# Kernel optimization log

Hardware: AMD Instinct MI355X
Metric: run time of the kernel (lower is better)

The kernel has to match this reference:

```python
import jax, jax.numpy as jnp
import numpy as np

NUM_HIDDENS = 512
NUM_HEADS = 4
B, S = 4, 2048


def setup_inputs() -> dict:
    key = jax.random.key(0)
    ks = jax.random.split(key, 10)
    H = NUM_HIDDENS
    scale = 1.0 / np.sqrt(H)
    return {
        "queries": jax.random.normal(ks[0], (B, S, H), jnp.float32),
        "keys": jax.random.normal(ks[1], (B, S, H), jnp.float32),
        "values": jax.random.normal(ks[2], (B, S, H), jnp.float32),
        "attention_mask": jax.random.randint(ks[3], (B, S), 0, 2).astype(bool),
        "Wq": jax.random.normal(ks[4], (H, H), jnp.float32) * scale,
        "bq": jnp.zeros((H,), jnp.float32),
        "Wk": jax.random.normal(ks[5], (H, H), jnp.float32) * scale,
        "bk": jnp.zeros((H,), jnp.float32),
        "Wv": jax.random.normal(ks[6], (H, H), jnp.float32) * scale,
        "bv": jnp.zeros((H,), jnp.float32),
    }


def reference(queries, keys, values, attention_mask, Wq, bq, Wk, bk, Wv, bv):
    B_, S_, H = queries.shape
    nh = NUM_HEADS
    dh = H // nh

    # QKV projections with ReLU (as in the original Sequential(Linear, ReLU))
    q = jax.nn.relu(jnp.einsum("bsh,oh->bso", queries, Wq) + bq)
    k = jax.nn.relu(jnp.einsum("bsh,oh->bso", keys, Wk) + bk)
    v = jax.nn.relu(jnp.einsum("bsh,oh->bso", values, Wv) + bv)

    # chunk along last dim + stack dim=1  ==  reshape [B,S,nh,dh] -> [B,nh,S,dh]
    qs = q.reshape(B_, S_, nh, dh).transpose(0, 2, 1, 3)
    ks_ = k.reshape(B_, S_, nh, dh).transpose(0, 2, 1, 3)
    vs = v.reshape(B_, S_, nh, dh).transpose(0, 2, 1, 3)

    # scores [B, nh, S, S]
    score = jnp.einsum("bhqd,bhkd->bhqk", qs, ks_) / jnp.sqrt(jnp.float32(dh))

    # 'enc' mask: [B,S] -> [B,1,S,1], fills entire QUERY rows (faithful quirk)
    row_mask = attention_mask[:, None, :, None]
    score = jnp.where(row_mask, jnp.float32(-1e9), score)

    attn = jax.nn.softmax(score, axis=-1)
    a = jnp.einsum("bhqk,bhkd->bhqd", attn, vs)  # [B, nh, S, dh]

    # faithful quirk: permute(0,1,3,2) then reshape to (B, S, H)
    a = jnp.transpose(a, (0, 1, 3, 2)).reshape(B_, S_, H)
    return a + queries
```

## Files before the change

### kernel.cpp

```cpp
#include <hip/hip_runtime.h>
#include <hip/hip_bf16.h>

typedef __attribute__((ext_vector_type(8)))  __bf16 bf16x8;
typedef __attribute__((ext_vector_type(4)))  __bf16 bf16x4;
typedef __attribute__((ext_vector_type(2)))  __bf16 bf16x2;
typedef __attribute__((ext_vector_type(4)))  float  f32x4;
typedef __attribute__((ext_vector_type(16))) float  f32x16;

#define MFMA16(a,b,c) __builtin_amdgcn_mfma_f32_16x16x32_bf16((a),(b),(c),0,0,0)
#define MFMA32(a,b,c) __builtin_amdgcn_mfma_f32_32x32x16_bf16((a),(b),(c),0,0,0)

__global__ __launch_bounds__(256, 2) void gemm_kernel(
    const float* __restrict__ Xq, const float* __restrict__ Xk,
    const float* __restrict__ Xv, const float* __restrict__ Wq,
    const float* __restrict__ Wk, const float* __restrict__ Wv,
    const float* __restrict__ bq, const float* __restrict__ bk,
    const float* __restrict__ bv, const int* __restrict__ mask,
    __bf16* __restrict__ dq, __bf16* __restrict__ dk, __bf16* __restrict__ dv)
{
  const int which = blockIdx.z;
  const float* X    = which == 0 ? Xq : which == 1 ? Xk : Xv;
  const float* W    = which == 0 ? Wq : which == 1 ? Wk : Wv;
  const float* bias = which == 0 ? bq : which == 1 ? bk : bv;
  __bf16* dst       = which == 0 ? dq : which == 1 ? dk : dv;
  const float oscale = which == 0 ? 0.12751744710339033f : 1.0f;

  __shared__ __align__(16) __bf16 Al[2][128 * 64];
  __shared__ __align__(16) __bf16 Bl[2][128 * 64];

  const int tid  = threadIdx.x;
  const int lane = tid & 63;
  const int w    = tid >> 6;
  const int wr = w >> 1, wc = w & 1;
  const int mbase = blockIdx.x * 128;
  const int nbase = blockIdx.y * 128;
  const int arow = lane & 15;
  const int hi   = lane >> 4;

  f32x4 acc[4][4] = {};
  float4 ar[8], br[8];

  auto issue = [&](int k0) {
#pragma unroll
    for (int i = 0; i < 8; ++i) {
      int idx = tid + i * 256;
      int r = idx >> 4, c = (idx & 15) * 4;
      ar[i] = *(const float4*)&X[(size_t)(mbase + r) * 512 + k0 + c];
      br[i] = *(const float4*)&W[(size_t)(nbase + r) * 512 + k0 + c];
    }
  };
  auto commit = [&](int buf) {
#pragma unroll
    for (int i = 0; i < 8; ++i) {
      int idx = tid + i * 256;
      int r = idx >> 4, c4 = idx & 15;
      int slot = c4 >> 1, half = c4 & 1;
      int addr = r * 64 + (slot ^ (r & 7)) * 8 + half * 4;
      bf16x4 av, bv2;
      av[0] = (__bf16)ar[i].x; av[1] = (__bf16)ar[i].y;
      av[2] = (__bf16)ar[i].z; av[3] = (__bf16)ar[i].w;
      bv2[0] = (__bf16)br[i].x; bv2[1] = (__bf16)br[i].y;
      bv2[2] = (__bf16)br[i].z; bv2[3] = (__bf16)br[i].w;
      *(bf16x4*)&Al[buf][addr] = av;
      *(bf16x4*)&Bl[buf][addr] = bv2;
    }
  };

  issue(0);
  commit(0);

  for (int t = 0; t < 8; ++t) {
    const int cur = t & 1;
    if (t < 7) issue((t + 1) * 64);
    __syncthreads();

    __builtin_amdgcn_s_setprio(1);
#pragma unroll
    for (int kk = 0; kk < 2; ++kk) {
      bf16x8 af[4], bfr[4];
#pragma unroll
      for (int m = 0; m < 4; ++m) {
        int row = wr * 64 + m * 16 + arow;
        int sl  = ((kk * 4 + hi) ^ (row & 7)) * 8;
        af[m] = *(bf16x8*)&Al[cur][row * 64 + sl];
      }
#pragma unroll
      for (int n = 0; n < 4; ++n) {
        int row = wc * 64 + n * 16 + arow;
        int sl  = ((kk * 4 + hi) ^ (row & 7)) * 8;
        bfr[n] = *(bf16x8*)&Bl[cur][row * 64 + sl];
      }
#pragma unroll
      for (int m = 0; m < 4; ++m)
#pragma unroll
        for (int n = 0; n < 4; ++n)
          acc[m][n] = MFMA16(af[m], bfr[n], acc[m][n]);
    }
    __builtin_amdgcn_s_setprio(0);

    if (t < 7) commit(cur ^ 1);
  }

#pragma unroll
  for (int n = 0; n < 4; ++n) {
    int col = nbase + wc * 64 + n * 16 + arow;
    float bsv = bias[col];
    int h = col >> 7, d = col & 127;
#pragma unroll
    for (int m = 0; m < 4; ++m) {
      int row0 = mbase + wr * 64 + m * 16 + hi * 4;
#pragma unroll
      for (int r = 0; r < 4; ++r) {
        float v = acc[m][n][r] + bsv;
        v = (v > 0.0f ? v : 0.0f) * oscale;
        int mm = row0 + r;
        int b = mm >> 11, s = mm & 2047;
        if (which == 0 && mask[b * 2048 + s] != 0) v = 0.0f;
        size_t bhoff = (size_t)(b * 4 + h) * (2048 * 128);
        int tt = s >> 6, kw_ = (s >> 5) & 1;
        if (which == 0) {
          dst[bhoff + (size_t)s * 128 + d] = (__bf16)v;
        } else if (which == 1) {
          int r5k = s & 31;
          int ds = d >> 4, hi3 = (d >> 3) & 1, j = d & 7;
          size_t unit = ((size_t)tt * 2 + kw_) * 8 + ds;
          dst[bhoff + unit * 512 + hi3 * 256 + r5k * 8 + j] = (__bf16)v;
        } else {
          int s2 = (s >> 4) & 1, hi3 = (s >> 3) & 1, j = s & 7;
          int dblk = d >> 5, r5 = d & 31;
          size_t unit = ((size_t)tt * 2 + kw_) * 8 + dblk * 2 + s2;
          dst[bhoff + unit * 512 + hi3 * 256 + r5 * 8 + j] = (__bf16)v;
        }
      }
    }
  }
}

__global__ __launch_bounds__(512, 2) void attn_kernel(
    const __bf16* __restrict__ qh, const __bf16* __restrict__ kfr,
    const __bf16* __restrict__ vfr, const float* __restrict__ queries,
    float* __restrict__ out)
{
  __shared__ float Ll[4][32];
  __shared__ __align__(16) float Ob[4][64 * 68];

  const int tid  = threadIdx.x;
  const int lane = tid & 63;
  const int w    = tid >> 6;
  const int qw   = w >> 1;
  const int kw   = w & 1;
  const int r5   = lane & 31;
  const int hi32 = lane >> 5;

  const int blk  = blockIdx.x;
  const int xcd  = blk & 7;
  const int rest = blk >> 3;
  const int bh   = xcd * 2 + (rest & 1);
  const int qt   = rest >> 1;
  const int b = bh >> 2, h = bh & 3;
  const int qbase = qt * 128 + qw * 32;

  const __bf16* qptr = qh  + (size_t)bh * 2048 * 128;
  const __bf16* kp   = kfr + (size_t)bh * 2048 * 128;
  const __bf16* vp   = vfr + (size_t)bh * 2048 * 128;

  bf16x8 qf[8];
#pragma unroll
  for (int ds = 0; ds < 8; ++ds)
    qf[ds] = *(const bf16x8*)&qptr[(size_t)(qbase + r5) * 128 + ds * 16 + hi32 * 8];

  float l_st = 0.f;
  f32x16 oacc[4] = {};
  bf16x8 kf[8], vfA[8], vfB[8];

  auto loadK = [&](int t) {
#pragma unroll
    for (int ds = 0; ds < 8; ++ds)
      kf[ds] = *(const bf16x8*)
          &kp[(((size_t)t * 2 + kw) * 8 + ds) * 512 + lane * 8];
  };
  auto loadV = [&](bf16x8 (&dstv)[8], int t) {
#pragma unroll
    for (int u = 0; u < 8; ++u)
      dstv[u] = *(const bf16x8*)
          &vp[(((size_t)t * 2 + kw) * 8 + u) * 512 + lane * 8];
  };

  auto body = [&](int t, bf16x8 (&vcur)[8]) {
    f32x16 sacc = {};
    __builtin_amdgcn_s_setprio(1);
#pragma unroll
    for (int ds = 0; ds < 8; ++ds)
      sacc = MFMA32(kf[ds], qf[ds], sacc);
    __builtin_amdgcn_s_setprio(0);

    if (t + 1 < 32) loadK(t + 1);

    float ps[16];
#pragma unroll
    for (int r = 0; r < 16; ++r) {
      ps[r] = __builtin_amdgcn_exp2f(sacc[r]);
      sacc[r] = ps[r];
    }
#pragma unroll
    for (int st = 1; st < 16; st <<= 1)
#pragma unroll
      for (int r = 0; r < 16; r += 2 * st)
        ps[r] += ps[r + st];
    l_st += ps[0];

    unsigned pk[8];
#pragma unroll
    for (int g = 0; g < 8; ++g) {
      bf16x2 tp;
      tp[0] = (__bf16)sacc[2 * g];
      tp[1] = (__bf16)sacc[2 * g + 1];
      pk[g] = __builtin_bit_cast(unsigned, tp);
    }
    bf16x8 pf[2];
#pragma unroll
    for (int s = 0; s < 2; ++s) {
      unsigned a0 = pk[4 * s + 0], a1 = pk[4 * s + 1];
      unsigned b0 = pk[4 * s + 2], b1 = pk[4 * s + 3];
      asm("v_permlane32_swap_b32 %0, %1" : "+v"(a0), "+v"(b0));
      asm("v_permlane32_swap_b32 %0, %1" : "+v"(a1), "+v"(b1));
      union { unsigned u[4]; bf16x8 v; } pu;
      pu.u[0] = a0; pu.u[1] = a1; pu.u[2] = b0; pu.u[3] = b1;
      pf[s] = pu.v;
    }

    __builtin_amdgcn_s_setprio(1);
#pragma unroll
    for (int u = 0; u < 8; ++u)
      oacc[u >> 1] = MFMA32(vcur[u], pf[u & 1], oacc[u >> 1]);
    __builtin_amdgcn_s_setprio(0);

    if (t + 2 < 32) loadV(vcur, t + 2);
  };

  loadK(0);
  loadV(vfA, 0);
  loadV(vfB, 1);

  for (int tt = 0; tt < 16; ++tt) {
    body(2 * tt, vfA);
    body(2 * tt + 1, vfB);
  }

  float l_tot = l_st + __shfl_xor(l_st, 32);

  if (kw == 1) {
    if (hi32 == 0) Ll[qw][r5] = l_tot;
    float* dstp = &Ob[qw][(size_t)lane * 68];
#pragma unroll
    for (int dblk = 0; dblk < 4; ++dblk)
      *(f32x16*)(dstp + dblk * 16) = oacc[dblk];
  }
  __syncthreads();

  if (kw == 0) {
    float l1 = Ll[qw][r5];
    float inv = 1.0f / (l_tot + l1);
    const float* src = &Ob[qw][(size_t)lane * 68];

    const int qq  = qt * 128 + qw * 32;
    const int qhi = qq >> 9;
    const int col = (qq & 511) + r5;
#pragma unroll
    for (int dblk = 0; dblk < 4; ++dblk) {
      f32x16 o1 = *(const f32x16*)(src + dblk * 16);
#pragma unroll
      for (int r = 0; r < 16; ++r) {
        int d = dblk * 32 + (r & 3) + 8 * (r >> 2) + 4 * hi32;
        int srow = h * 512 + d * 4 + qhi;
        size_t o = ((size_t)b * 2048 + srow) * 512 + col;
        out[o] = (oacc[dblk][r] + o1[r]) * inv + queries[o];
      }
    }
  }
}

extern "C" void kernel_launch(void* const* d_in, const int* in_sizes, int n_in,
                              void* d_out, int out_size, void* d_ws, size_t ws_size,
                              hipStream_t stream) {
  const float* queries = (const float*)d_in[0];
  const float* keys    = (const float*)d_in[1];
  const float* values  = (const float*)d_in[2];
  const int*   mask    = (const int*)d_in[3];
  const float* Wq = (const float*)d_in[4];
  const float* bq = (const float*)d_in[5];
  const float* Wk = (const float*)d_in[6];
  const float* bk = (const float*)d_in[7];
  const float* Wv = (const float*)d_in[8];
  const float* bv = (const float*)d_in[9];
  float* out = (float*)d_out;

  const size_t perX = (size_t)8192 * 512;
  __bf16* qhp = (__bf16*)d_ws;
  __bf16* khp = qhp + perX;
  __bf16* vtp = khp + perX;

  gemm_kernel<<<dim3(64, 4, 3), dim3(256), 0, stream>>>(
      queries, keys, values, Wq, Wk, Wv, bq, bk, bv, mask, qhp, khp, vtp);

  attn_kernel<<<dim3(256), dim3(512), 0, stream>>>(qhp, khp, vtp, queries, out);
}
```

Baseline: 86.59 us.

## Switch attention to 16x16 MFMA with smaller query tiles and halve GEMM K-tile

The attention kernel moves from 32x32x16 MFMA with 128-query blocks of 512 threads to 16x16x32 MFMA with 32-query blocks of 256 threads, launching four times as many blocks. The K/V fragment layouts written by the projection GEMM change to match, and the P matrix is redistributed with lane shuffles instead of permlane32 swaps. The GEMM K-tile is halved to 32 with a new LDS swizzle, which lowers LDS use and register pressure but doubles the number of barrier iterations. Smaller attention tiles raise occupancy and parallelism, but each K/V element is now re-read from global memory four times as often, and the shuffles cost more than the permlane swaps.

```diff
diff --git a/kernel.cpp b/kernel.cpp
--- a/kernel.cpp
+++ b/kernel.cpp
@@ -5,10 +5,8 @@
 typedef __attribute__((ext_vector_type(4)))  __bf16 bf16x4;
 typedef __attribute__((ext_vector_type(2)))  __bf16 bf16x2;
 typedef __attribute__((ext_vector_type(4)))  float  f32x4;
-typedef __attribute__((ext_vector_type(16))) float  f32x16;
 
 #define MFMA16(a,b,c) __builtin_amdgcn_mfma_f32_16x16x32_bf16((a),(b),(c),0,0,0)
-#define MFMA32(a,b,c) __builtin_amdgcn_mfma_f32_32x32x16_bf16((a),(b),(c),0,0,0)
 
 __global__ __launch_bounds__(256, 2) void gemm_kernel(
     const float* __restrict__ Xq, const float* __restrict__ Xk,
@@ -25,8 +23,8 @@
   __bf16* dst       = which == 0 ? dq : which == 1 ? dk : dv;
   const float oscale = which == 0 ? 0.12751744710339033f : 1.0f;
 
-  __shared__ __align__(16) __bf16 Al[2][128 * 64];
-  __shared__ __align__(16) __bf16 Bl[2][128 * 64];
+  __shared__ __align__(16) __bf16 Al[2][128 * 32];
+  __shared__ __align__(16) __bf16 Bl[2][128 * 32];
 
   const int tid  = threadIdx.x;
   const int lane = tid & 63;
@@ -38,24 +36,24 @@
   const int hi   = lane >> 4;
 
   f32x4 acc[4][4] = {};
-  float4 ar[8], br[8];
+  float4 ar[4], br[4];
 
   auto issue = [&](int k0) {
 #pragma unroll
-    for (int i = 0; i < 8; ++i) {
+    for (int i = 0; i < 4; ++i) {
       int idx = tid + i * 256;
-      int r = idx >> 4, c = (idx & 15) * 4;
+      int r = idx >> 3, c = (idx & 7) * 4;
       ar[i] = *(const float4*)&X[(size_t)(mbase + r) * 512 + k0 + c];
       br[i] = *(const float4*)&W[(size_t)(nbase + r) * 512 + k0 + c];
     }
   };
   auto commit = [&](int buf) {
 #pragma unroll
-    for (int i = 0; i < 8; ++i) {
+    for (int i = 0; i < 4; ++i) {
       int idx = tid + i * 256;
-      int r = idx >> 4, c4 = idx & 15;
-      int slot = c4 >> 1, half = c4 & 1;
-      int addr = r * 64 + (slot ^ (r & 7)) * 8 + half * 4;
+      int r = idx >> 3, c = (idx & 7) * 4;
+      int slot = c >> 3, half = (c >> 2) & 1;
+      int addr = r * 32 + (((slot + (r >> 2)) & 3) ^ (r & 3)) * 8 + half * 4;
       bf16x4 av, bv2;
       av[0] = (__bf16)ar[i].x; av[1] = (__bf16)ar[i].y;
       av[2] = (__bf16)ar[i].z; av[3] = (__bf16)ar[i].w;
@@ -69,26 +67,25 @@
   issue(0);
   commit(0);
 
-  for (int t = 0; t < 8; ++t) {
+  for (int t = 0; t < 16; ++t) {
     const int cur = t & 1;
-    if (t < 7) issue((t + 1) * 64);
+    if (t < 15) issue((t + 1) * 32);
     __syncthreads();
 
     __builtin_amdgcn_s_setprio(1);
-#pragma unroll
-    for (int kk = 0; kk < 2; ++kk) {
+    {
       bf16x8 af[4], bfr[4];
 #pragma unroll
       for (int m = 0; m < 4; ++m) {
         int row = wr * 64 + m * 16 + arow;
-        int sl  = ((kk * 4 + hi) ^ (row & 7)) * 8;
-        af[m] = *(bf16x8*)&Al[cur][row * 64 + sl];
+        int sl  = (((hi + (row >> 2)) & 3) ^ (row & 3)) * 8;
+        af[m] = *(bf16x8*)&Al[cur][row * 32 + sl];
       }
 #pragma unroll
       for (int n = 0; n < 4; ++n) {
         int row = wc * 64 + n * 16 + arow;
-        int sl  = ((kk * 4 + hi) ^ (row & 7)) * 8;
-        bfr[n] = *(bf16x8*)&Bl[cur][row * 64 + sl];
+        int sl  = (((hi + (row >> 2)) & 3) ^ (row & 3)) * 8;
+        bfr[n] = *(bf16x8*)&Bl[cur][row * 32 + sl];
       }
 #pragma unroll
       for (int m = 0; m < 4; ++m)
@@ -98,14 +95,14 @@
     }
     __builtin_amdgcn_s_setprio(0);
 
-    if (t < 7) commit(cur ^ 1);
+    if (t < 15) commit(cur ^ 1);
   }
 
 #pragma unroll
   for (int n = 0; n < 4; ++n) {
     int col = nbase + wc * 64 + n * 16 + arow;
     float bsv = bias[col];
-    int h = col >> 7, d = col & 127;
+    int hd = col >> 7, d = col & 127;
 #pragma unroll
     for (int m = 0; m < 4; ++m) {
       int row0 = mbase + wr * 64 + m * 16 + hi * 4;
@@ -116,165 +113,162 @@
         int mm = row0 + r;
         int b = mm >> 11, s = mm & 2047;
         if (which == 0 && mask[b * 2048 + s] != 0) v = 0.0f;
-        size_t bhoff = (size_t)(b * 4 + h) * (2048 * 128);
-        int tt = s >> 6, kw_ = (s >> 5) & 1;
+        size_t bhoff = (size_t)(b * 4 + hd) * (2048 * 128);
         if (which == 0) {
           dst[bhoff + (size_t)s * 128 + d] = (__bf16)v;
         } else if (which == 1) {
-          int r5k = s & 31;
-          int ds = d >> 4, hi3 = (d >> 3) & 1, j = d & 7;
-          size_t unit = ((size_t)tt * 2 + kw_) * 8 + ds;
-          dst[bhoff + unit * 512 + hi3 * 256 + r5k * 8 + j] = (__bf16)v;
+          size_t unit = (size_t)(s >> 5) * 8 + ((s >> 4) & 1) * 4 + (d >> 5);
+          dst[bhoff + unit * 512 + (s & 15) * 8 + ((d & 31) >> 3) * 128 +
+              (d & 7)] = (__bf16)v;
         } else {
-          int s2 = (s >> 4) & 1, hi3 = (s >> 3) & 1, j = s & 7;
-          int dblk = d >> 5, r5 = d & 31;
-          size_t unit = ((size_t)tt * 2 + kw_) * 8 + dblk * 2 + s2;
-          dst[bhoff + unit * 512 + hi3 * 256 + r5 * 8 + j] = (__bf16)v;
+          size_t unit = (size_t)(s >> 5) * 8 + (d >> 4);
+          dst[bhoff + unit * 512 + (d & 15) * 8 + ((s & 31) >> 3) * 128 +
+              (s & 7)] = (__bf16)v;
         }
       }
     }
   }
 }
 
-__global__ __launch_bounds__(512, 2) void attn_kernel(
+__global__ __launch_bounds__(256) void attn_kernel(
     const __bf16* __restrict__ qh, const __bf16* __restrict__ kfr,
     const __bf16* __restrict__ vfr, const float* __restrict__ queries,
     float* __restrict__ out)
 {
-  __shared__ float Ll[4][32];
-  __shared__ __align__(16) float Ob[4][64 * 68];
+  __shared__ float Ml[2][16];
+  __shared__ __align__(16) float Ob[2 * 8 * 256];
 
   const int tid  = threadIdx.x;
   const int lane = tid & 63;
   const int w    = tid >> 6;
-  const int qw   = w >> 1;
-  const int kw   = w & 1;
-  const int r5   = lane & 31;
-  const int hi32 = lane >> 5;
+  const int qw   = w & 1;
+  const int kw   = w >> 1;
+  const int q16  = lane & 15;
+  const int hi4  = lane >> 4;
 
   const int blk  = blockIdx.x;
   const int xcd  = blk & 7;
   const int rest = blk >> 3;
   const int bh   = xcd * 2 + (rest & 1);
   const int qt   = rest >> 1;
-  const int b = bh >> 2, h = bh & 3;
-  const int qbase = qt * 128 + qw * 32;
+  const int b = bh >> 2, hd = bh & 3;
+  const int qbase = qt * 32 + qw * 16;
 
   const __bf16* qptr = qh  + (size_t)bh * 2048 * 128;
   const __bf16* kp   = kfr + (size_t)bh * 2048 * 128;
   const __bf16* vp   = vfr + (size_t)bh * 2048 * 128;
 
-  bf16x8 qf[8];
-#pragma unroll
-  for (int ds = 0; ds < 8; ++ds)
-    qf[ds] = *(const bf16x8*)&qptr[(size_t)(qbase + r5) * 128 + ds * 16 + hi32 * 8];
+  bf16x8 qf[4];
+#pragma unroll
+  for (int sl = 0; sl < 4; ++sl)
+    qf[sl] = *(const bf16x8*)
+        &qptr[(size_t)(qbase + q16) * 128 + sl * 32 + hi4 * 8];
+
+  const int srcA = q16 + (((2 * hi4) & 3) << 4);
+  const int srcB = q16 + (((2 * hi4 + 1) & 3) << 4);
+  const bool selhi = hi4 >= 2;
 
   float l_st = 0.f;
-  f32x16 oacc[4] = {};
-  bf16x8 kf[8], vfA[8], vfB[8];
-
-  auto loadK = [&](int t) {
-#pragma unroll
-    for (int ds = 0; ds < 8; ++ds)
-      kf[ds] = *(const bf16x8*)
-          &kp[(((size_t)t * 2 + kw) * 8 + ds) * 512 + lane * 8];
+  f32x4 oacc[8] = {};
+  bf16x8 kf[2][4], vf[8];
+
+  auto loadK = [&](int i) {
+    size_t cb = (size_t)(i * 2 + kw) * 8 * 512;
+#pragma unroll
+    for (int hh = 0; hh < 2; ++hh)
+#pragma unroll
+      for (int sl = 0; sl < 4; ++sl)
+        kf[hh][sl] = *(const bf16x8*)
+            &kp[cb + (size_t)(hh * 4 + sl) * 512 + lane * 8];
   };
-  auto loadV = [&](bf16x8 (&dstv)[8], int t) {
-#pragma unroll
-    for (int u = 0; u < 8; ++u)
-      dstv[u] = *(const bf16x8*)
-          &vp[(((size_t)t * 2 + kw) * 8 + u) * 512 + lane * 8];
+  auto loadV = [&](int i) {
+    size_t cb = (size_t)(i * 2 + kw) * 8 * 512;
+#pragma unroll
+    for (int dt = 0; dt < 8; ++dt)
+      vf[dt] = *(const bf16x8*)&vp[cb + (size_t)dt * 512 + lane * 8];
   };
 
-  auto body = [&](int t, bf16x8 (&vcur)[8]) {
-    f32x16 sacc = {};
+  loadK(0);
+  loadV(0);
+
+  for (int i = 0; i < 32; ++i) {
+    f32x4 s0 = {}, s1 = {};
     __builtin_amdgcn_s_setprio(1);
 #pragma unroll
-    for (int ds = 0; ds < 8; ++ds)
-      sacc = MFMA32(kf[ds], qf[ds], sacc);
+    for (int sl = 0; sl < 4; ++sl) s0 = MFMA16(kf[0][sl], qf[sl], s0);
+#pragma unroll
+    for (int sl = 0; sl < 4; ++sl) s1 = MFMA16(kf[1][sl], qf[sl], s1);
     __builtin_amdgcn_s_setprio(0);
 
-    if (t + 1 < 32) loadK(t + 1);
-
-    float ps[16];
-#pragma unroll
-    for (int r = 0; r < 16; ++r) {
-      ps[r] = __builtin_amdgcn_exp2f(sacc[r]);
-      sacc[r] = ps[r];
-    }
-#pragma unroll
-    for (int st = 1; st < 16; st <<= 1)
-#pragma unroll
-      for (int r = 0; r < 16; r += 2 * st)
-        ps[r] += ps[r + st];
-    l_st += ps[0];
-
-    unsigned pk[8];
-#pragma unroll
-    for (int g = 0; g < 8; ++g) {
-      bf16x2 tp;
-      tp[0] = (__bf16)sacc[2 * g];
-      tp[1] = (__bf16)sacc[2 * g + 1];
-      pk[g] = __builtin_bit_cast(unsigned, tp);
-    }
-    bf16x8 pf[2];
-#pragma unroll
-    for (int s = 0; s < 2; ++s) {
-      unsigned a0 = pk[4 * s + 0], a1 = pk[4 * s + 1];
-      unsigned b0 = pk[4 * s + 2], b1 = pk[4 * s + 3];
-      asm("v_permlane32_swap_b32 %0, %1" : "+v"(a0), "+v"(b0));
-      asm("v_permlane32_swap_b32 %0, %1" : "+v"(a1), "+v"(b1));
-      union { unsigned u[4]; bf16x8 v; } pu;
-      pu.u[0] = a0; pu.u[1] = a1; pu.u[2] = b0; pu.u[3] = b1;
-      pf[s] = pu.v;
-    }
+    if (i + 1 < 32) loadK(i + 1);
+
+    float p0[4], p1[4];
+#pragma unroll
+    for (int r = 0; r < 4; ++r) {
+      p0[r] = __builtin_amdgcn_exp2f(s0[r]);
+      p1[r] = __builtin_amdgcn_exp2f(s1[r]);
+    }
+    l_st += ((p0[0] + p0[1]) + (p0[2] + p0[3])) +
+            ((p1[0] + p1[1]) + (p1[2] + p1[3]));
+
+    unsigned pk0[2], pk1[2];
+    {
+      bf16x2 t0, t1, t2, t3;
+      t0[0] = (__bf16)p0[0]; t0[1] = (__bf16)p0[1];
+      t1[0] = (__bf16)p0[2]; t1[1] = (__bf16)p0[3];
+      t2[0] = (__bf16)p1[0]; t2[1] = (__bf16)p1[1];
+      t3[0] = (__bf16)p1[2]; t3[1] = (__bf16)p1[3];
+      pk0[0] = __builtin_bit_cast(unsigned, t0);
+      pk0[1] = __builtin_bit_cast(unsigned, t1);
+      pk1[0] = __builtin_bit_cast(unsigned, t2);
+      pk1[1] = __builtin_bit_cast(unsigned, t3);
+    }
+    unsigned w0a = __shfl(pk0[0], srcA), w0b = __shfl(pk1[0], srcA);
+    unsigned w1a = __shfl(pk0[1], srcA), w1b = __shfl(pk1[1], srcA);
+    unsigned w2a = __shfl(pk0[0], srcB), w2b = __shfl(pk1[0], srcB);
+    unsigned w3a = __shfl(pk0[1], srcB), w3b = __shfl(pk1[1], srcB);
+    union { unsigned u[4]; bf16x8 v; } pu;
+    pu.u[0] = selhi ? w0b : w0a;
+    pu.u[1] = selhi ? w1b : w1a;
+    pu.u[2] = selhi ? w2b : w2a;
+    pu.u[3] = selhi ? w3b : w3a;
+    bf16x8 pf = pu.v;
 
     __builtin_amdgcn_s_setprio(1);
 #pragma unroll
-    for (int u = 0; u < 8; ++u)
-      oacc[u >> 1] = MFMA32(vcur[u], pf[u & 1], oacc[u >> 1]);
+    for (int dt = 0; dt < 8; ++dt)
+      oacc[dt] = MFMA16(vf[dt], pf, oacc[dt]);
     __builtin_amdgcn_s_setprio(0);
 
-    if (t + 2 < 32) loadV(vcur, t + 2);
-  };
-
-  loadK(0);
-  loadV(vfA, 0);
-  loadV(vfB, 1);
-
-  for (int tt = 0; tt < 16; ++tt) {
-    body(2 * tt, vfA);
-    body(2 * tt + 1, vfB);
-  }
-
-  float l_tot = l_st + __shfl_xor(l_st, 32);
-
+    if (i + 1 < 32) loadV(i + 1);
+  }
+
+  l_st += __shfl_xor(l_st, 16);
+  l_st += __shfl_xor(l_st, 32);
+
+  __syncthreads();
   if (kw == 1) {
-    if (hi32 == 0) Ll[qw][r5] = l_tot;
-    float* dstp = &Ob[qw][(size_t)lane * 68];
-#pragma unroll
-    for (int dblk = 0; dblk < 4; ++dblk)
-      *(f32x16*)(dstp + dblk * 16) = oacc[dblk];
+    if (lane < 16) Ml[qw][lane] = l_st;
+#pragma unroll
+    for (int dt = 0; dt < 8; ++dt)
+      *(f32x4*)&Ob[(qw * 8 + dt) * 256 + lane * 4] = oacc[dt];
   }
   __syncthreads();
 
   if (kw == 0) {
-    float l1 = Ll[qw][r5];
-    float inv = 1.0f / (l_tot + l1);
-    const float* src = &Ob[qw][(size_t)lane * 68];
-
-    const int qq  = qt * 128 + qw * 32;
-    const int qhi = qq >> 9;
-    const int col = (qq & 511) + r5;
-#pragma unroll
-    for (int dblk = 0; dblk < 4; ++dblk) {
-      f32x16 o1 = *(const f32x16*)(src + dblk * 16);
-#pragma unroll
-      for (int r = 0; r < 16; ++r) {
-        int d = dblk * 32 + (r & 3) + 8 * (r >> 2) + 4 * hi32;
-        int srow = h * 512 + d * 4 + qhi;
+    float inv = 1.0f / (l_st + Ml[qw][q16]);
+    const int qg = qbase + q16;
+    const int qhi = qg >> 9;
+    const int col = qg & 511;
+#pragma unroll
+    for (int dt = 0; dt < 8; ++dt) {
+      f32x4 o1 = *(const f32x4*)&Ob[(qw * 8 + dt) * 256 + lane * 4];
+#pragma unroll
+      for (int r = 0; r < 4; ++r) {
+        int d = dt * 16 + hi4 * 4 + r;
+        int srow = hd * 512 + d * 4 + qhi;
         size_t o = ((size_t)b * 2048 + srow) * 512 + col;
-        out[o] = (oacc[dblk][r] + o1[r]) * inv + queries[o];
+        out[o] = (oacc[dt][r] + o1[r]) * inv + queries[o];
       }
     }
   }
@@ -303,5 +297,5 @@
   gemm_kernel<<<dim3(64, 4, 3), dim3(256), 0, stream>>>(
       queries, keys, values, Wq, Wk, Wv, bq, bk, bv, mask, qhp, khp, vtp);
 
-  attn_kernel<<<dim3(256), dim3(512), 0, stream>>>(qhp, khp, vtp, queries, out);
+  attn_kernel<<<dim3(1024), dim3(256), 0, stream>>>(qhp, khp, vtp, queries, out);
 }
```

New measurement: 104.8 us. 1.21x slower.
